# Optimization experiments

Measured on AMD Instinct MI355X. Metric: run time of the kernel, lower is better.

## Reference

```python
import jax, jax.numpy as jnp
import numpy as np

B, T, N, U = 16, 512, 2048, 64  # batch_size, dim1, dim2 (=nodes), units


def setup_inputs() -> dict:
    key = jax.random.key(0)
    k1, k2, k3, k4 = jax.random.split(key, 4)
    x = jax.random.normal(k1, (B, T, N), dtype=jnp.float32)
    Adj = jax.random.uniform(k2, (N, N), dtype=jnp.float32)
    W = jax.random.normal(k3, (U, N), dtype=jnp.float32) * 0.05  # 'uniform' init stand-in
    b = jax.random.normal(k4, (U,), dtype=jnp.float32) * 0.05
    return {"x": x, "Adj": Adj, "W": W, "b": b}


def reference(x, Adj, W, b):
    # Original loop: out_i[b,t,j] = sum_k x[b,t,k] * Adj[j,k] * W[i,k] + b[i],
    # then mean over i. By linearity this equals a single matmul with the
    # unit-averaged weight vector and the averaged bias.
    w_bar = jnp.mean(W, axis=0)              # [N]
    w_eff = Adj * w_bar                       # [N(j), N(k)] : Adj[j,k] * w_bar[k]
    out = jnp.einsum('btk,jk->btj', x, w_eff) + jnp.mean(b)
    return out  # [B, T, N]
```

## Files before the change

kernel.cpp:

```cpp
#include <hip/hip_runtime.h>

#define N_DIM 2048
#define U_DIM 64
#define M_DIM 8192
#define K_DIM 2048

typedef __bf16 bf16x8 __attribute__((ext_vector_type(8)));
typedef float  floatx4 __attribute__((ext_vector_type(4)));
typedef float  floatx16 __attribute__((ext_vector_type(16)));
typedef unsigned short ushort8 __attribute__((ext_vector_type(8)));

#define AS1 __attribute__((address_space(1)))
#define AS3 __attribute__((address_space(3)))

__device__ __forceinline__ unsigned short f_to_bf16_rne(float f) {
    unsigned int x;
    __builtin_memcpy(&x, &f, 4);
    x += 0x7fffu + ((x >> 16) & 1u);
    return (unsigned short)(x >> 16);
}

__global__ __launch_bounds__(256) void prep_kernel(
    const float* __restrict__ W, const float* __restrict__ b,
    float* __restrict__ wbar, float* __restrict__ bmean) {
    int k = blockIdx.x * 256 + threadIdx.x;
    float s = 0.f;
#pragma unroll
    for (int i = 0; i < U_DIM; ++i) s += W[i * N_DIM + k];
    wbar[k] = s * (1.f / U_DIM);

    if (blockIdx.x == 0 && threadIdx.x < 64) {
        float v = b[threadIdx.x];
#pragma unroll
        for (int off = 32; off > 0; off >>= 1) v += __shfl_down(v, off);
        if (threadIdx.x == 0) bmean[0] = v * (1.f / U_DIM);
    }
}

__global__ __launch_bounds__(256) void weff_convx_kernel(
    const float* __restrict__ Adj, const float* __restrict__ wbar,
    unsigned short* __restrict__ weff,
    const float* __restrict__ x, unsigned short* __restrict__ xbf) {
    if (blockIdx.x < 2048) {
        long long idx = ((long long)blockIdx.x * 256 + threadIdx.x) * 8;
        int k = (int)(idx & (N_DIM - 1));
        floatx4 a0 = *(const floatx4*)(Adj + idx);
        floatx4 a1 = *(const floatx4*)(Adj + idx + 4);
        floatx4 w0 = *(const floatx4*)(wbar + k);
        floatx4 w1 = *(const floatx4*)(wbar + k + 4);
        ushort8 ov;
#pragma unroll
        for (int j = 0; j < 4; ++j) {
            ov[j]     = f_to_bf16_rne(a0[j] * w0[j]);
            ov[j + 4] = f_to_bf16_rne(a1[j] * w1[j]);
        }
        *(ushort8*)(weff + idx) = ov;
    } else {
        long long idx = ((long long)(blockIdx.x - 2048) * 256 + threadIdx.x) * 8;
        floatx4 a0 = *(const floatx4*)(x + idx);
        floatx4 a1 = *(const floatx4*)(x + idx + 4);
        ushort8 ov;
#pragma unroll
        for (int j = 0; j < 4; ++j) {
            ov[j]     = f_to_bf16_rne(a0[j]);
            ov[j + 4] = f_to_bf16_rne(a1[j]);
        }
        *(ushort8*)(xbf + idx) = ov;
    }
}

__global__ __launch_bounds__(256) void convx_kernel(
    const float* __restrict__ x, unsigned short* __restrict__ xbf) {
    long long idx = ((long long)blockIdx.x * 256 + threadIdx.x) * 8;
    floatx4 a0 = *(const floatx4*)(x + idx);
    floatx4 a1 = *(const floatx4*)(x + idx + 4);
    ushort8 ov;
#pragma unroll
    for (int j = 0; j < 4; ++j) {
        ov[j]     = f_to_bf16_rne(a0[j]);
        ov[j + 4] = f_to_bf16_rne(a1[j]);
    }
    *(ushort8*)(xbf + idx) = ov;
}

#define BM 256
#define BN 256
#define BK 64
#define NT (K_DIM / BK)

__global__ __launch_bounds__(512, 2) void gemm_bt_kernel(
    const unsigned short* __restrict__ A,
    const unsigned short* __restrict__ Bt,
    const float* __restrict__ bmeanp,
    float* __restrict__ C,
    int mtiles) {
    __shared__ __align__(16) unsigned short sA[2][BM * BK];
    __shared__ __align__(16) unsigned short sB[2][BN * BK];

    const int id   = blockIdx.x;
    const int nt   = id & 7;
    const int mt   = id >> 3;
    const int tile_m = mt * BM;
    const int tile_n = nt * BN;

    const int tid  = threadIdx.x;
    const int w    = tid >> 6;
    const int lane = tid & 63;
    const int wm   = w >> 2;
    const int wn   = w & 3;

    const float bmean = bmeanp[0];

    const int srow = lane >> 3;
    const int skc  = (lane & 7) ^ srow;
    const unsigned short* gA0 = A  + (size_t)(tile_m + w * 32 + srow) * K_DIM + skc * 8;
    const unsigned short* gB0 = Bt + (size_t)(tile_n + w * 32 + srow) * K_DIM + skc * 8;

    const int ln31 = lane & 31;
    const int hq   = lane >> 5;
    const int l7   = lane & 7;
    int abase[4], bbase[2], slotk[4];
#pragma unroll
    for (int mi = 0; mi < 4; ++mi) abase[mi] = (wm * 128 + mi * 32 + ln31) * BK;
#pragma unroll
    for (int ni = 0; ni < 2; ++ni) bbase[ni] = (wn * 64 + ni * 32 + ln31) * BK;
#pragma unroll
    for (int s = 0; s < 4; ++s)    slotk[s] = ((s * 2 + hq) ^ l7) * 8;

    floatx16 acc[4][2];
#pragma unroll
    for (int mi = 0; mi < 4; ++mi)
#pragma unroll
        for (int ni = 0; ni < 2; ++ni)
#pragma unroll
            for (int r = 0; r < 16; ++r) acc[mi][ni][r] = 0.f;

    #define STAGE(p, kt)                                                          \
        do {                                                                      \
            const int koff_ = (kt) * BK;                                          \
            _Pragma("unroll")                                                     \
            for (int i_ = 0; i_ < 4; ++i_) {                                      \
                __builtin_amdgcn_global_load_lds(                                 \
                    (const AS1 void*)(gA0 + koff_ + (size_t)i_ * 8 * K_DIM),      \
                    (AS3 void*)(&sA[(p)][(w * 4 + i_) * 8 * BK]), 16, 0, 0);      \
                __builtin_amdgcn_global_load_lds(                                 \
                    (const AS1 void*)(gB0 + koff_ + (size_t)i_ * 8 * K_DIM),      \
                    (AS3 void*)(&sB[(p)][(w * 4 + i_) * 8 * BK]), 16, 0, 0);      \
            }                                                                     \
        } while (0)

    STAGE(0, 0);
    STAGE(1, 1);

    for (int t = 0; t < NT; ++t) {
        const int p = t & 1;

        if (t == NT - 1) asm volatile("s_waitcnt vmcnt(0)" ::: "memory");
        else             asm volatile("s_waitcnt vmcnt(8)" ::: "memory");
        __builtin_amdgcn_s_barrier();

        bf16x8 b01[2][2], b23[2][2], a0[4], a1[4], a2[4], a3[4];

#pragma unroll
        for (int ni = 0; ni < 2; ++ni)
#pragma unroll
            for (int s = 0; s < 2; ++s)
                b01[ni][s] = *(const bf16x8*)&sB[p][bbase[ni] + slotk[s]];
#pragma unroll
        for (int mi = 0; mi < 4; ++mi)
            a0[mi] = *(const bf16x8*)&sA[p][abase[mi] + slotk[0]];
        __builtin_amdgcn_sched_barrier(0);

#pragma unroll
        for (int mi = 0; mi < 4; ++mi)
            a1[mi] = *(const bf16x8*)&sA[p][abase[mi] + slotk[1]];
#pragma unroll
        for (int ni = 0; ni < 2; ++ni)
#pragma unroll
            for (int s = 0; s < 2; ++s)
                b23[ni][s] = *(const bf16x8*)&sB[p][bbase[ni] + slotk[2 + s]];
        __builtin_amdgcn_sched_barrier(0);
        __builtin_amdgcn_s_setprio(1);
#pragma unroll
        for (int mi = 0; mi < 4; ++mi)
#pragma unroll
            for (int ni = 0; ni < 2; ++ni)
                acc[mi][ni] = __builtin_amdgcn_mfma_f32_32x32x16_bf16(
                    a0[mi], b01[ni][0], acc[mi][ni], 0, 0, 0);
        __builtin_amdgcn_s_setprio(0);

#pragma unroll
        for (int mi = 0; mi < 4; ++mi)
            a2[mi] = *(const bf16x8*)&sA[p][abase[mi] + slotk[2]];
        __builtin_amdgcn_sched_barrier(0);
        __builtin_amdgcn_s_setprio(1);
#pragma unroll
        for (int mi = 0; mi < 4; ++mi)
#pragma unroll
            for (int ni = 0; ni < 2; ++ni)
                acc[mi][ni] = __builtin_amdgcn_mfma_f32_32x32x16_bf16(
                    a1[mi], b01[ni][1], acc[mi][ni], 0, 0, 0);
        __builtin_amdgcn_s_setprio(0);

#pragma unroll
        for (int mi = 0; mi < 4; ++mi)
            a3[mi] = *(const bf16x8*)&sA[p][abase[mi] + slotk[3]];
        __builtin_amdgcn_sched_barrier(0);
        __builtin_amdgcn_s_setprio(1);
#pragma unroll
        for (int mi = 0; mi < 4; ++mi)
#pragma unroll
            for (int ni = 0; ni < 2; ++ni)
                acc[mi][ni] = __builtin_amdgcn_mfma_f32_32x32x16_bf16(
                    a2[mi], b23[ni][0], acc[mi][ni], 0, 0, 0);
        __builtin_amdgcn_s_setprio(0);

        asm volatile("s_waitcnt lgkmcnt(0)" ::: "memory");
        __builtin_amdgcn_sched_barrier(0);
        __builtin_amdgcn_s_barrier();
        if (t + 2 < NT) STAGE(p, t + 2);
        __builtin_amdgcn_sched_barrier(0);
        __builtin_amdgcn_s_setprio(1);
#pragma unroll
        for (int mi = 0; mi < 4; ++mi)
#pragma unroll
            for (int ni = 0; ni < 2; ++ni)
                acc[mi][ni] = __builtin_amdgcn_mfma_f32_32x32x16_bf16(
                    a3[mi], b23[ni][1], acc[mi][ni], 0, 0, 0);
        __builtin_amdgcn_s_setprio(0);
    }
    #undef STAGE

    const int crow = tile_m + wm * 128 + hq * 4;
    const int ccol = tile_n + wn * 64 + ln31;
#pragma unroll
    for (int mi = 0; mi < 4; ++mi)
#pragma unroll
        for (int ni = 0; ni < 2; ++ni)
#pragma unroll
            for (int r = 0; r < 16; ++r) {
                int gm = crow + mi * 32 + (r & 3) + 8 * (r >> 2);
                int gn = ccol + ni * 32;
                C[(size_t)gm * N_DIM + gn] = acc[mi][ni][r] + bmean;
            }
    (void)mtiles;
}

extern "C" void kernel_launch(void* const* d_in, const int* in_sizes, int n_in,
                              void* d_out, int out_size, void* d_ws, size_t ws_size,
                              hipStream_t stream) {
    (void)in_sizes; (void)n_in; (void)out_size;
    const float* x   = (const float*)d_in[0];
    const float* Adj = (const float*)d_in[1];
    const float* W   = (const float*)d_in[2];
    const float* b   = (const float*)d_in[3];
    float* out = (float*)d_out;

    char* ws = (char*)d_ws;
    float* wbar  = (float*)ws;
    float* bmean = (float*)(ws + 8192);
    unsigned short* weff = (unsigned short*)(ws + 16384);
    const size_t weff_bytes = (size_t)N_DIM * N_DIM * 2;
    const size_t xbf_off = 16384 + weff_bytes;
    unsigned short* xbf = (unsigned short*)(ws + xbf_off);

    size_t avail = (ws_size > xbf_off) ? (ws_size - xbf_off) : 0;
    long long max_rows = (long long)(avail / ((size_t)K_DIM * 2)) / BM * BM;
    if (max_rows < BM) max_rows = BM;
    if (max_rows > M_DIM) max_rows = M_DIM;

    prep_kernel<<<N_DIM / 256, 256, 0, stream>>>(W, b, wbar, bmean);

    if (max_rows == M_DIM) {
        weff_convx_kernel<<<2048 + M_DIM, 256, 0, stream>>>(Adj, wbar, weff, x, xbf);
        gemm_bt_kernel<<<(M_DIM / BM) * (N_DIM / BN), 512, 0, stream>>>(
            xbf, weff, bmean, out, M_DIM / BM);
    } else {
        weff_convx_kernel<<<2048, 256, 0, stream>>>(Adj, wbar, weff, x, xbf);
        for (long long m0 = 0; m0 < M_DIM; m0 += max_rows) {
            long long rows = (M_DIM - m0 < max_rows) ? (M_DIM - m0) : max_rows;
            convx_kernel<<<(int)rows, 256, 0, stream>>>(x + m0 * K_DIM, xbf);
            gemm_bt_kernel<<<(int)(rows / BM) * (N_DIM / BN), 512, 0, stream>>>(
                xbf, weff, bmean, out + m0 * (size_t)N_DIM, (int)(rows / BM));
        }
    }
}
```

Before: 219.9 us.

## Fuse x fp32-to-bf16 conversion into GEMM A-tile loading

Removes the separate x conversion pass and bf16 staging buffer. The GEMM now loads fp32 x tiles into registers, converts them to bf16 and writes them to swizzled LDS, while B still uses direct global-to-LDS loads. This saves a full read/write pass over x but doubles the A-operand global traffic per tile and adds register pressure and extra wait points in the pipeline.

```diff
diff --git a/kernel.cpp b/kernel.cpp
--- a/kernel.cpp
+++ b/kernel.cpp
@@ -9,6 +9,7 @@
 typedef float  floatx4 __attribute__((ext_vector_type(4)));
 typedef float  floatx16 __attribute__((ext_vector_type(16)));
 typedef unsigned short ushort8 __attribute__((ext_vector_type(8)));
+typedef unsigned short ushort4b __attribute__((ext_vector_type(4)));
 
 #define AS1 __attribute__((address_space(1)))
 #define AS3 __attribute__((address_space(3)))
@@ -37,50 +38,22 @@
     }
 }
 
-__global__ __launch_bounds__(256) void weff_convx_kernel(
+__global__ __launch_bounds__(256) void weff_kernel(
     const float* __restrict__ Adj, const float* __restrict__ wbar,
-    unsigned short* __restrict__ weff,
-    const float* __restrict__ x, unsigned short* __restrict__ xbf) {
-    if (blockIdx.x < 2048) {
-        long long idx = ((long long)blockIdx.x * 256 + threadIdx.x) * 8;
-        int k = (int)(idx & (N_DIM - 1));
-        floatx4 a0 = *(const floatx4*)(Adj + idx);
-        floatx4 a1 = *(const floatx4*)(Adj + idx + 4);
-        floatx4 w0 = *(const floatx4*)(wbar + k);
-        floatx4 w1 = *(const floatx4*)(wbar + k + 4);
-        ushort8 ov;
-#pragma unroll
-        for (int j = 0; j < 4; ++j) {
-            ov[j]     = f_to_bf16_rne(a0[j] * w0[j]);
-            ov[j + 4] = f_to_bf16_rne(a1[j] * w1[j]);
-        }
-        *(ushort8*)(weff + idx) = ov;
-    } else {
-        long long idx = ((long long)(blockIdx.x - 2048) * 256 + threadIdx.x) * 8;
-        floatx4 a0 = *(const floatx4*)(x + idx);
-        floatx4 a1 = *(const floatx4*)(x + idx + 4);
-        ushort8 ov;
-#pragma unroll
-        for (int j = 0; j < 4; ++j) {
-            ov[j]     = f_to_bf16_rne(a0[j]);
-            ov[j + 4] = f_to_bf16_rne(a1[j]);
-        }
-        *(ushort8*)(xbf + idx) = ov;
+    unsigned short* __restrict__ weff) {
+    long long idx = ((long long)blockIdx.x * 256 + threadIdx.x) * 8;
+    int k = (int)(idx & (N_DIM - 1));
+    floatx4 a0 = *(const floatx4*)(Adj + idx);
+    floatx4 a1 = *(const floatx4*)(Adj + idx + 4);
+    floatx4 w0 = *(const floatx4*)(wbar + k);
+    floatx4 w1 = *(const floatx4*)(wbar + k + 4);
+    ushort8 ov;
+#pragma unroll
+    for (int j = 0; j < 4; ++j) {
+        ov[j]     = f_to_bf16_rne(a0[j] * w0[j]);
+        ov[j + 4] = f_to_bf16_rne(a1[j] * w1[j]);
     }
-}
-
-__global__ __launch_bounds__(256) void convx_kernel(
-    const float* __restrict__ x, unsigned short* __restrict__ xbf) {
-    long long idx = ((long long)blockIdx.x * 256 + threadIdx.x) * 8;
-    floatx4 a0 = *(const floatx4*)(x + idx);
-    floatx4 a1 = *(const floatx4*)(x + idx + 4);
-    ushort8 ov;
-#pragma unroll
-    for (int j = 0; j < 4; ++j) {
-        ov[j]     = f_to_bf16_rne(a0[j]);
-        ov[j + 4] = f_to_bf16_rne(a1[j]);
-    }
-    *(ushort8*)(xbf + idx) = ov;
+    *(ushort8*)(weff + idx) = ov;
 }
 
 #define BM 256
@@ -89,7 +62,7 @@
 #define NT (K_DIM / BK)
 
 __global__ __launch_bounds__(512, 2) void gemm_bt_kernel(
-    const unsigned short* __restrict__ A,
+    const float* __restrict__ X,
     const unsigned short* __restrict__ Bt,
     const float* __restrict__ bmeanp,
     float* __restrict__ C,
@@ -113,8 +86,14 @@
 
     const int srow = lane >> 3;
     const int skc  = (lane & 7) ^ srow;
-    const unsigned short* gA0 = A  + (size_t)(tile_m + w * 32 + srow) * K_DIM + skc * 8;
     const unsigned short* gB0 = Bt + (size_t)(tile_n + w * 32 + srow) * K_DIM + skc * 8;
+
+    const int arow = lane >> 3;
+    const int acq  = lane & 7;
+    const float* gX = X + (size_t)(tile_m + w * 32 + arow) * K_DIM + acq * 4;
+    const unsigned awbase = (w * 32 + arow) * BK;
+    const unsigned awoff0 = (((acq >> 1)     ^ arow) * 8u) + (acq & 1) * 4u;
+    const unsigned awoff1 = (((4 + (acq >> 1)) ^ arow) * 8u) + (acq & 1) * 4u;
 
     const int ln31 = lane & 31;
     const int hq   = lane >> 5;
@@ -135,29 +114,64 @@
 #pragma unroll
             for (int r = 0; r < 16; ++r) acc[mi][ni][r] = 0.f;
 
-    #define STAGE(p, kt)                                                          \
+    #define STAGE_B(p, kt)                                                        \
         do {                                                                      \
             const int koff_ = (kt) * BK;                                          \
             _Pragma("unroll")                                                     \
             for (int i_ = 0; i_ < 4; ++i_) {                                      \
                 __builtin_amdgcn_global_load_lds(                                 \
-                    (const AS1 void*)(gA0 + koff_ + (size_t)i_ * 8 * K_DIM),      \
-                    (AS3 void*)(&sA[(p)][(w * 4 + i_) * 8 * BK]), 16, 0, 0);      \
-                __builtin_amdgcn_global_load_lds(                                 \
                     (const AS1 void*)(gB0 + koff_ + (size_t)i_ * 8 * K_DIM),      \
                     (AS3 void*)(&sB[(p)][(w * 4 + i_) * 8 * BK]), 16, 0, 0);      \
             }                                                                     \
         } while (0)
 
-    STAGE(0, 0);
-    STAGE(1, 1);
+    #define AGLD(AV, kt)                                                          \
+        do {                                                                      \
+            _Pragma("unroll")                                                     \
+            for (int c_ = 0; c_ < 4; ++c_) {                                      \
+                AV[c_][0] = *(const floatx4*)(gX + (kt) * BK +                    \
+                                              (size_t)c_ * 8 * K_DIM);            \
+                AV[c_][1] = *(const floatx4*)(gX + (kt) * BK +                    \
+                                              (size_t)c_ * 8 * K_DIM + 32);       \
+            }                                                                     \
+        } while (0)
+
+    #define AWRITE(p, AV)                                                         \
+        do {                                                                      \
+            _Pragma("unroll")                                                     \
+            for (int c_ = 0; c_ < 4; ++c_) {                                      \
+                ushort4b t0_, t1_;                                                \
+                _Pragma("unroll")                                                 \
+                for (int j_ = 0; j_ < 4; ++j_) {                                  \
+                    t0_[j_] = f_to_bf16_rne(AV[c_][0][j_]);                       \
+                    t1_[j_] = f_to_bf16_rne(AV[c_][1][j_]);                       \
+                }                                                                 \
+                *(ushort4b*)&sA[(p)][awbase + c_ * 8 * BK + awoff0] = t0_;        \
+                *(ushort4b*)&sA[(p)][awbase + c_ * 8 * BK + awoff1] = t1_;        \
+            }                                                                     \
+        } while (0)
+
+    floatx4 av0[4][2], av1[4][2], av[4][2];
+    AGLD(av0, 0);
+    AGLD(av1, 1);
+    STAGE_B(0, 0);
+    STAGE_B(1, 1);
+    asm volatile("s_waitcnt vmcnt(16)" ::: "memory");
+    __builtin_amdgcn_sched_barrier(0);
+    AWRITE(0, av0);
+    asm volatile("s_waitcnt vmcnt(8)" ::: "memory");
+    __builtin_amdgcn_sched_barrier(0);
+    AWRITE(1, av1);
+    asm volatile("s_waitcnt vmcnt(4)" ::: "memory");
+    asm volatile("s_waitcnt lgkmcnt(0)" ::: "memory");
 
     for (int t = 0; t < NT; ++t) {
         const int p = t & 1;
 
-        if (t == NT - 1) asm volatile("s_waitcnt vmcnt(0)" ::: "memory");
-        else             asm volatile("s_waitcnt vmcnt(8)" ::: "memory");
         __builtin_amdgcn_s_barrier();
+
+        if (t + 2 < NT) AGLD(av, t + 2);
+        __builtin_amdgcn_sched_barrier(0);
 
         bf16x8 b01[2][2], b23[2][2], a0[4], a1[4], a2[4], a3[4];
 
@@ -218,7 +232,12 @@
         asm volatile("s_waitcnt lgkmcnt(0)" ::: "memory");
         __builtin_amdgcn_sched_barrier(0);
         __builtin_amdgcn_s_barrier();
-        if (t + 2 < NT) STAGE(p, t + 2);
+        asm volatile("s_waitcnt vmcnt(0)" ::: "memory");
+        __builtin_amdgcn_sched_barrier(0);
+        if (t + 2 < NT) {
+            AWRITE(p, av);
+            STAGE_B(p, t + 2);
+        }
         __builtin_amdgcn_sched_barrier(0);
         __builtin_amdgcn_s_setprio(1);
 #pragma unroll
@@ -228,8 +247,11 @@
                 acc[mi][ni] = __builtin_amdgcn_mfma_f32_32x32x16_bf16(
                     a3[mi], b23[ni][1], acc[mi][ni], 0, 0, 0);
         __builtin_amdgcn_s_setprio(0);
+        asm volatile("s_waitcnt lgkmcnt(0)" ::: "memory");
     }
-    #undef STAGE
+    #undef STAGE_B
+    #undef AGLD
+    #undef AWRITE
 
     const int crow = tile_m + wm * 128 + hq * 4;
     const int ccol = tile_n + wn * 64 + ln31;
@@ -249,7 +271,7 @@
 extern "C" void kernel_launch(void* const* d_in, const int* in_sizes, int n_in,
                               void* d_out, int out_size, void* d_ws, size_t ws_size,
                               hipStream_t stream) {
-    (void)in_sizes; (void)n_in; (void)out_size;
+    (void)in_sizes; (void)n_in; (void)out_size; (void)ws_size;
     const float* x   = (const float*)d_in[0];
     const float* Adj = (const float*)d_in[1];
     const float* W   = (const float*)d_in[2];
@@ -260,28 +282,9 @@
     float* wbar  = (float*)ws;
     float* bmean = (float*)(ws + 8192);
     unsigned short* weff = (unsigned short*)(ws + 16384);
-    const size_t weff_bytes = (size_t)N_DIM * N_DIM * 2;
-    const size_t xbf_off = 16384 + weff_bytes;
-    unsigned short* xbf = (unsigned short*)(ws + xbf_off);
-
-    size_t avail = (ws_size > xbf_off) ? (ws_size - xbf_off) : 0;
-    long long max_rows = (long long)(avail / ((size_t)K_DIM * 2)) / BM * BM;
-    if (max_rows < BM) max_rows = BM;
-    if (max_rows > M_DIM) max_rows = M_DIM;
 
     prep_kernel<<<N_DIM / 256, 256, 0, stream>>>(W, b, wbar, bmean);
-
-    if (max_rows == M_DIM) {
-        weff_convx_kernel<<<2048 + M_DIM, 256, 0, stream>>>(Adj, wbar, weff, x, xbf);
-        gemm_bt_kernel<<<(M_DIM / BM) * (N_DIM / BN), 512, 0, stream>>>(
-            xbf, weff, bmean, out, M_DIM / BM);
-    } else {
-        weff_convx_kernel<<<2048, 256, 0, stream>>>(Adj, wbar, weff, x, xbf);
-        for (long long m0 = 0; m0 < M_DIM; m0 += max_rows) {
-            long long rows = (M_DIM - m0 < max_rows) ? (M_DIM - m0) : max_rows;
-            convx_kernel<<<(int)rows, 256, 0, stream>>>(x + m0 * K_DIM, xbf);
-            gemm_bt_kernel<<<(int)(rows / BM) * (N_DIM / BN), 512, 0, stream>>>(
-                xbf, weff, bmean, out + m0 * (size_t)N_DIM, (int)(rows / BM));
-        }
-    }
-}
+    weff_kernel<<<2048, 256, 0, stream>>>(Adj, wbar, weff);
+    gemm_bt_kernel<<<(M_DIM / BM) * (N_DIM / BN), 512, 0, stream>>>(
+        x, weff, bmean, out, M_DIM / BM);
+}
```

After: 231.4 us. 5.2% more time.
